# Performance work log

Hardware: AMD Instinct MI355X
Metric: run time of the kernel (lower is better)

The kernel has to match this reference:

```python
import jax, jax.numpy as jnp
import numpy as np

N, E, B = 128000, 512000, 128

def _conv1d(x, w, b):
    # x: [B,C,L], w: [O,I,K] (torch layout) -> valid conv, stride 1
    y = jax.lax.conv_general_dilated(x, w, (1,), 'VALID',
                                     dimension_numbers=('NCH', 'OIH', 'NCH'))
    return y + b[None, :, None]

def setup_inputs():
    key = jax.random.key(0)
    ks = jax.random.split(key, 22)
    def u(k, shape, fan_in):
        bound = 1.0 / np.sqrt(fan_in)
        return jax.random.uniform(k, shape, jnp.float32, -bound, bound)
    x = jax.random.normal(ks[0], (N, 33), jnp.float32)
    edge_index = jax.random.randint(ks[1], (2, E), 0, N, dtype=jnp.int64)
    batch = (jnp.arange(N, dtype=jnp.int64) * B) // N  # sorted, every graph non-empty
    target = jax.random.normal(ks[2], (B, 26, 1000), jnp.float32)
    return {
        'x': x, 'edge_index': edge_index, 'batch': batch, 'target': target,
        'lin_w': u(ks[3], (256, 33), 33), 'lin_b': jnp.zeros((256,), jnp.float32),
        'conv1_w': u(ks[4], (64, 26, 3), 26 * 3), 'conv1_b': u(ks[5], (64,), 26 * 3),
        'conv2_w': u(ks[6], (256, 64, 3), 64 * 3), 'conv2_b': u(ks[7], (256,), 64 * 3),
        'conv3_w': u(ks[8], (1024, 256, 5), 256 * 5), 'conv3_b': u(ks[9], (1024,), 256 * 5),
        'fc_w': u(ks[10], (768, 1024), 1024), 'fc_b': u(ks[11], (768,), 1024),
        'm1_w': u(ks[12], (1024, 1024), 1024), 'm1_b': u(ks[13], (1024,), 1024),
        'm2_w': u(ks[14], (1024, 1024), 1024), 'm2_b': u(ks[15], (1024,), 1024),
        'm3_w': u(ks[16], (512, 1024), 1024), 'm3_b': u(ks[17], (512,), 1024),
        'm4_w': u(ks[18], (1, 512), 512), 'm4_b': u(ks[19], (1,), 512),
    }

def reference(x, edge_index, batch, target,
              lin_w, lin_b, conv1_w, conv1_b, conv2_w, conv2_b,
              conv3_w, conv3_b, fc_w, fc_b,
              m1_w, m1_b, m2_w, m2_b, m3_w, m3_b, m4_w, m4_b):
    # ---- drug branch: GCN-normalized message passing, sum-aggr, graph mean ----
    xw = x @ lin_w.T                                   # [N,256]
    row, col = edge_index[0], edge_index[1]            # source j, target i
    deg = jax.ops.segment_sum(jnp.ones((E,), x.dtype), col, num_segments=N)
    dis = jnp.where(deg > 0, deg ** -0.5, 0.0)
    norm = dis[row] * dis[col]                         # [E]
    agg = jax.ops.segment_sum(norm[:, None] * xw[row], col, num_segments=N)
    out = agg + lin_b                                  # [N,256]
    sums = jax.ops.segment_sum(out, batch, num_segments=B)
    cnt = jax.ops.segment_sum(jnp.ones((N,), x.dtype), batch, num_segments=B)
    drug = jnp.where(cnt[:, None] > 0, sums / cnt[:, None], 0.0)  # [B,256]
    # ---- target branch: CNN (dropout = identity in eval) ----
    h = jax.nn.relu(_conv1d(target, conv1_w, conv1_b))
    h = jax.nn.relu(_conv1d(h, conv2_w, conv2_b))
    h = jax.nn.relu(_conv1d(h, conv3_w, conv3_b))
    h = jnp.max(h, axis=2)                             # AdaptiveMaxPool1d(1) -> [B,1024]
    tgt = jax.nn.relu(h @ fc_w.T + fc_b)               # [B,768]
    # ---- head MLP ----
    z = jnp.concatenate([drug, tgt], axis=1)           # [B,1024]
    z = jax.nn.relu(z @ m1_w.T + m1_b)
    z = jax.nn.relu(z @ m2_w.T + m2_b)
    z = jax.nn.relu(z @ m3_w.T + m3_b)
    return z @ m4_w.T + m4_b                           # [B,1]
```

## Files before the change

### kernel.cpp

```cpp
#include <hip/hip_runtime.h>

typedef unsigned short u16;
typedef __attribute__((ext_vector_type(8))) short short8;
typedef __attribute__((ext_vector_type(4))) float f32x4;

#define NN 128000
#define EE 512000
#define GB 128

#define GLDS16(g, l)                                                     \
  __builtin_amdgcn_global_load_lds(                                      \
      (const __attribute__((address_space(1))) unsigned int*)(g),        \
      (__attribute__((address_space(3))) unsigned int*)(l), 16, 0, 0)

__device__ __forceinline__ float u2f(u16 u) {
  union { unsigned u32; float f; } v; v.u32 = ((unsigned)u) << 16; return v.f;
}
__device__ __forceinline__ u16 f2bf(float x) {
  union { float f; unsigned u; } v; v.f = x;
  unsigned r = v.u + 0x7FFF + ((v.u >> 16) & 1);
  return (u16)(r >> 16);
}

__global__ void k_transpose(const float* w1, const float* w2, const float* w3,
                            float* w1T, u16* w2t, u16* w3p) {
  int idx = blockIdx.x * 256 + threadIdx.x;
  if (idx < 4992) { int o = idx & 63, ck = idx >> 6; w1T[idx] = w1[o * 78 + ck]; return; }
  idx -= 4992;
  if (idx < 49152) {
    int c = idx & 63, o = (idx >> 6) & 255, k = idx >> 14;
    w2t[idx] = f2bf(w2[o * 192 + c * 3 + k]);
    return;
  }
  idx -= 49152;
  if (idx < 1310720) {
    int stcbk = idx >> 15;
    int fi    = (idx >> 9) & 63;
    int r512  = idx & 511;
    int quad  = r512 >> 7, l16 = (r512 >> 3) & 15, i = r512 & 7;
    int stcb  = stcbk / 5, k = stcbk - stcb * 5;
    int o = fi * 16 + l16;
    int c = stcb * 32 + quad * 8 + i;
    w3p[idx] = f2bf(w3[o * 1280 + c * 5 + k]);
  }
}

__global__ void k_deg_start(const int* ei, const int* batch, int* deg, int* start, int* hist) {
  __shared__ int lh[GB];
  int tid = threadIdx.x, blk = blockIdx.x;
  if (tid < GB) lh[tid] = 0;
  __syncthreads();
  int e0 = blk * 1024;
#pragma unroll
  for (int t = 0; t < 4; t++) {
    int e = e0 + t * 256 + tid;
    int col = ei[EE + e];
    atomicAdd(&deg[col], 1);
    atomicAdd(&lh[batch[col]], 1);
  }
  int i = blk * 256 + tid;
  int b = batch[i];
  if (i == 0) start[0] = 0;
  else if (b != batch[i - 1]) start[b] = i;
  if (i == NN - 1) start[GB] = NN;
  __syncthreads();
  if (tid < GB && lh[tid]) atomicAdd(&hist[tid * 16], lh[tid]);
}

__global__ void k_prefix(const int* hist, int* off, int* cursor) {
  __shared__ int h[GB];
  int tid = threadIdx.x;
  h[tid] = hist[tid * 16];
  __syncthreads();
  int s = 0;
  for (int j = 0; j < tid; j++) s += h[j];
  off[tid] = s;
  cursor[tid * 16] = s;
  if (tid == GB - 1) off[GB] = s + h[GB - 1];
}

__global__ void k_scatter(const int* ei, const int* batch, const int* deg,
                          int* cursor, uint2* bucket) {
  __shared__ int lh[GB];
  __shared__ int lbase[GB];
  int tid = threadIdx.x, blk = blockIdx.x;
  if (tid < GB) lh[tid] = 0;
  __syncthreads();
  int e0 = blk * 1024;
  int row[4], g[4], rk[4]; float nrm[4];
#pragma unroll
  for (int t = 0; t < 4; t++) {
    int e = e0 + t * 256 + tid;
    int r = ei[e], c = ei[EE + e];
    row[t] = r;
    g[t] = batch[c];
    int dr = deg[r], dc = deg[c];
    float fr = dr > 0 ? rsqrtf((float)dr) : 0.f;
    float fc = dc > 0 ? rsqrtf((float)dc) : 0.f;
    nrm[t] = fr * fc;
    rk[t] = atomicAdd(&lh[g[t]], 1);
  }
  __syncthreads();
  if (tid < GB && lh[tid]) lbase[tid] = atomicAdd(&cursor[tid * 16], lh[tid]);
  __syncthreads();
#pragma unroll
  for (int t = 0; t < 4; t++) {
    uint2 v; v.x = (unsigned)row[t]; v.y = __float_as_uint(nrm[t]);
    bucket[lbase[g[t]] + rk[t]] = v;
  }
}

__global__ void k_gather33(const uint2* bucket, const int* off, const float* x, float* y) {
  __shared__ float red[4][33];
  int tid = threadIdx.x;
  int s = blockIdx.x, g = blockIdx.y;
  int lo = off[g], hi = off[g + 1];
  int cnt = hi - lo;
  int per = (cnt + 15) >> 4;
  int b0 = lo + s * per, b1 = min(b0 + per, hi);
  int lane = tid & 63, wid = tid >> 6;
  float acc = 0.f;
  if (lane < 33) {
#pragma unroll 4
    for (int e = b0 + wid; e < b1; e += 4) {
      uint2 be = bucket[e];
      float nrm = __uint_as_float(be.y);
      acc = fmaf(nrm, x[(size_t)be.x * 33 + lane], acc);
    }
    red[wid][lane] = acc;
  }
  __syncthreads();
  if (tid < 33) {
    float v = red[0][tid] + red[1][tid] + red[2][tid] + red[3][tid];
    if (v != 0.f) atomicAdd(&y[g * 33 + tid], v);
  }
}

__global__ void k_conv1(const float* target, const float* w1T, const float* b1, u16* h1T) {
  __shared__ float ts[26][132];
  __shared__ float wls[78 * 64];
  int tid = threadIdx.x, lt = blockIdx.x, bl = blockIdx.y;
  int l0 = lt * 128;
  int q = tid >> 6, lane = tid & 63;
  for (int c = q; c < 26; c += 4)
    for (int i = lane; i < 130; i += 64)
      ts[c][i] = target[(bl * 26 + c) * 1000 + min(l0 + i, 999)];
  for (int i = tid; i < 4992; i += 256) wls[i] = w1T[i];
  __syncthreads();
  int o = tid & 63, wid = tid >> 6;
  float w[78];
#pragma unroll
  for (int i = 0; i < 78; i++) w[i] = wls[i * 64 + o];
  float bias = b1[o];
  for (int t = 0; t < 32; t++) {
    int li = wid * 32 + t;
    float acc = bias;
#pragma unroll
    for (int c = 0; c < 26; c++)
#pragma unroll
      for (int k = 0; k < 3; k++) acc += ts[c][li + k] * w[c * 3 + k];
    int lg = l0 + li;
    if (lg < 998) h1T[((size_t)bl * 1000 + lg) * 64 + o] = f2bf(fmaxf(acc, 0.f));
  }
}

__global__ void k_conv2(const u16* h1T, const u16* w2t, const float* b2, u16* h2T) {
  __shared__ __align__(16) u16 als[132 * 32];
  __shared__ __align__(16) u16 bls[3 * 128 * 32];
  int tid = threadIdx.x;
  int lt = blockIdx.x, ot = blockIdx.y, bl = blockIdx.z;
  int l0 = lt * 128, o0 = ot * 128;
  int lane = tid & 63, wid = tid >> 6;
  int wm = wid >> 1, wn = wid & 1;
  int quad = lane >> 4, l16 = lane & 15;
  const f32x4 zero = {0.f, 0.f, 0.f, 0.f};
  f32x4 acc[4][4];
#pragma unroll
  for (int i = 0; i < 4; i++)
#pragma unroll
    for (int j = 0; j < 4; j++) acc[i][j] = zero;
  for (int cb = 0; cb < 2; cb++) {
    int c0 = cb * 32;
#pragma unroll
    for (int rr = 0; rr < 2; rr++) {
      int cid = rr * 256 + wid * 64 + lane;
      int row = cid >> 2, ch = (cid & 3) ^ (row & 3);
      GLDS16(h1T + ((size_t)bl * 1000 + min(l0 + row, 997)) * 64 + c0 + ch * 8,
             als + (rr * 256 + wid * 64) * 8);
    }
    if (wid == 0 && lane < 8) {
      int cid = 512 + lane;
      int row = cid >> 2, ch = (cid & 3) ^ (row & 3);
      GLDS16(h1T + ((size_t)bl * 1000 + min(l0 + row, 997)) * 64 + c0 + ch * 8, als + 512 * 8);
    }
#pragma unroll
    for (int rr = 0; rr < 6; rr++) {
      int cid = rr * 256 + wid * 64 + lane;
      int rko = cid >> 2, k = rko >> 7, o = rko & 127;
      int ch = (cid & 3) ^ (rko & 3);
      GLDS16(w2t + ((size_t)(k * 256 + o0 + o)) * 64 + c0 + ch * 8,
             bls + (rr * 256 + wid * 64) * 8);
    }
    __syncthreads();
#pragma unroll
    for (int k = 0; k < 3; k++) {
      short8 af[4], bfr[4];
#pragma unroll
      for (int i = 0; i < 4; i++) {
        int row = k + wm * 64 + i * 16 + l16;
        af[i] = *(const short8*)(als + row * 32 + ((quad ^ (row & 3)) * 8));
      }
#pragma unroll
      for (int j = 0; j < 4; j++) {
        int rowB = wn * 64 + j * 16 + l16;
        bfr[j] = *(const short8*)(bls + (k * 128 + rowB) * 32 + ((quad ^ (rowB & 3)) * 8));
      }
#pragma unroll
      for (int i = 0; i < 4; i++)
#pragma unroll
        for (int j = 0; j < 4; j++)
          acc[i][j] = __builtin_amdgcn_mfma_f32_16x16x32_bf16(af[i], bfr[j], acc[i][j], 0, 0, 0);
    }
    __syncthreads();
  }
#pragma unroll
  for (int j = 0; j < 4; j++) {
    int col = o0 + wn * 64 + j * 16 + l16;
    float bias = b2[col];
#pragma unroll
    for (int i = 0; i < 4; i++)
#pragma unroll
      for (int r = 0; r < 4; r++) {
        int lg = l0 + wm * 64 + i * 16 + quad * 4 + r;
        if (lg < 996)
          h2T[((size_t)bl * 996 + lg) * 256 + col] = f2bf(fmaxf(acc[i][j][r] + bias, 0.f));
      }
  }
}

__global__ void __launch_bounds__(256, 2)
k_conv3(const u16* h2T, const u16* w3p, const float* b3, float* pooledT) {
  __shared__ __align__(16) u16 als[2][1088 * 8];
  __shared__ float mbuf[256];
  int bid = blockIdx.x;
  int xc = bid & 7, rr0 = bid >> 3;
  int ot = rr0 & 3, bl = xc * 16 + (rr0 >> 2);
  int o0 = ot * 256;
  int tid = threadIdx.x;
  int lane = tid & 63, wn = tid >> 6;
  int quad = lane >> 4, l16 = lane & 15;
  float omax[4];
#pragma unroll
  for (int j = 0; j < 4; j++) omax[j] = -3.0e38f;
  const f32x4 zero = {0.f, 0.f, 0.f, 0.f};
  const u16* wb = w3p + (size_t)(ot * 16 + wn * 4) * 512 + lane * 8;
  const size_t rowbase = (size_t)bl * 996;

  {
    u16* dst = als[0];
#pragma unroll
    for (int c = 0; c < 4; c++) {
      int cid = c * 256 + tid;
      int row = cid >> 3, pp = cid & 7;
      int cc = (pp - row) & 7;
      GLDS16(h2T + (rowbase + min(row, 995)) * 256 + cc * 8, dst + cid * 8);
    }
    if (tid < 64) {
      int cid = 1024 + tid;
      int row = cid >> 3, pp = cid & 7;
      int cc = (pp - row) & 7;
      GLDS16(h2T + (rowbase + min(row, 995)) * 256 + cc * 8, dst + cid * 8);
    }
  }
  asm volatile("s_waitcnt vmcnt(0)" ::: "memory");
  __builtin_amdgcn_s_barrier();

  for (int lt = 0; lt < 8; lt++) {
    f32x4 acc[8][4];
#pragma unroll
    for (int i = 0; i < 8; i++)
#pragma unroll
      for (int j = 0; j < 4; j++) acc[i][j] = zero;
#pragma unroll 1
    for (int qc = 0; qc < 4; qc++) {
      const u16* a = als[qc & 1];
      {
        const u16* p_ = wb + (size_t)(qc * 2) * 5 * 32768;
        short8 breg[4];
        breg[0] = *(const short8*)(p_);
        breg[1] = *(const short8*)(p_ + 512);
        breg[2] = *(const short8*)(p_ + 1024);
        breg[3] = *(const short8*)(p_ + 1536);
#pragma unroll
        for (int i = 0; i < 8; i++) {
          int row = i * 16 + l16;
          int pp = (quad + row) & 7;
          short8 af = *(const short8*)(a + row * 64 + pp * 8);
          acc[i][0] = __builtin_amdgcn_mfma_f32_16x16x32_bf16(af, breg[0], acc[i][0], 0, 0, 0);
          acc[i][1] = __builtin_amdgcn_mfma_f32_16x16x32_bf16(af, breg[1], acc[i][1], 0, 0, 0);
          acc[i][2] = __builtin_amdgcn_mfma_f32_16x16x32_bf16(af, breg[2], acc[i][2], 0, 0, 0);
          acc[i][3] = __builtin_amdgcn_mfma_f32_16x16x32_bf16(af, breg[3], acc[i][3], 0, 0, 0);
        }
      }
      if (lt * 4 + qc < 31) {
        int nqc = (qc + 1) & 3;
        int nlt = lt + (qc == 3 ? 1 : 0);
        int l0n = nlt * 128;
        u16* dst = als[(qc + 1) & 1];
#pragma unroll
        for (int c = 0; c < 4; c++) {
          int cid = c * 256 + tid;
          int row = cid >> 3, pp = cid & 7;
          int cc = (pp - row) & 7;
          GLDS16(h2T + (rowbase + min(l0n + row, 995)) * 256 + nqc * 64 + cc * 8,
                 dst + cid * 8);
        }
        if (tid < 64) {
          int cid = 1024 + tid;
          int row = cid >> 3, pp = cid & 7;
          int cc = (pp - row) & 7;
          GLDS16(h2T + (rowbase + min(l0n + row, 995)) * 256 + nqc * 64 + cc * 8,
                 dst + cid * 8);
        }
      }
#pragma unroll 1
      for (int cbq = 0; cbq < 2; cbq++) {
        int stcb = qc * 2 + cbq;
        int k0 = (cbq == 0) ? 1 : 0;
#pragma unroll
        for (int k = k0; k < 5; k++) {
          const u16* p_ = wb + (size_t)(stcb * 5 + k) * 32768;
          short8 breg[4];
          breg[0] = *(const short8*)(p_);
          breg[1] = *(const short8*)(p_ + 512);
          breg[2] = *(const short8*)(p_ + 1024);
          breg[3] = *(const short8*)(p_ + 1536);
#pragma unroll
          for (int i = 0; i < 8; i++) {
            int row = k + i * 16 + l16;
            int pp = (cbq * 4 + quad + row) & 7;
            short8 af = *(const short8*)(a + row * 64 + pp * 8);
            acc[i][0] = __builtin_amdgcn_mfma_f32_16x16x32_bf16(af, breg[0], acc[i][0], 0, 0, 0);
            acc[i][1] = __builtin_amdgcn_mfma_f32_16x16x32_bf16(af, breg[1], acc[i][1], 0, 0, 0);
            acc[i][2] = __builtin_amdgcn_mfma_f32_16x16x32_bf16(af, breg[2], acc[i][2], 0, 0, 0);
            acc[i][3] = __builtin_amdgcn_mfma_f32_16x16x32_bf16(af, breg[3], acc[i][3], 0, 0, 0);
          }
        }
      }
      asm volatile("s_waitcnt vmcnt(0)" ::: "memory");
      __builtin_amdgcn_s_barrier();
    }
    int l0 = lt * 128;
#pragma unroll
    for (int i = 0; i < 8; i++) {
#pragma unroll
      for (int r = 0; r < 4; r++) {
        int lg = l0 + i * 16 + quad * 4 + r;
        if (lg < 992) {
#pragma unroll
          for (int j = 0; j < 4; j++) omax[j] = fmaxf(omax[j], acc[i][j][r]);
        }
      }
    }
  }
#pragma unroll
  for (int j = 0; j < 4; j++) {
    omax[j] = fmaxf(omax[j], __shfl_xor(omax[j], 16, 64));
    omax[j] = fmaxf(omax[j], __shfl_xor(omax[j], 32, 64));
  }
  if (quad == 0) {
#pragma unroll
    for (int j = 0; j < 4; j++) mbuf[wn * 64 + j * 16 + l16] = omax[j];
  }
  __syncthreads();
  {
    float v = mbuf[tid] + b3[o0 + tid];
    pooledT[(size_t)(o0 + tid) * 128 + bl] = fmaxf(v, 0.f);
  }
}

__global__ void k_z0(const float* y, const int* start, const float* lin_w, const float* lin_b,
                     const float* tgtT, float* z0T) {
  int idx = blockIdx.x * 256 + threadIdx.x;
  int r = idx >> 7, bb = idx & 127;
  float v;
  if (r < 256) {
    float cnt = (float)(start[bb + 1] - start[bb]);
    const float* yr = y + bb * 33;
    const float* wr = lin_w + r * 33;
    float acc = 0.f;
#pragma unroll
    for (int i = 0; i < 33; i++) acc = fmaf(yr[i], wr[i], acc);
    v = acc / cnt + lin_b[r];
  } else {
    v = tgtT[(r - 256) * 128 + bb];
  }
  z0T[idx] = v;
}

__global__ void k_fc4(const float* zT, const float* W, const float* bias, float* outT,
                      int K, int O) {
  __shared__ float wls[4 * 1024];
  int tid = threadIdx.x;
  int o0 = blockIdx.x * 4;
  for (int idx = tid; idx < 4 * K; idx += 512) {
    int oo = idx / K, i = idx - oo * K;
    wls[oo * K + i] = W[(size_t)(o0 + oo) * K + i];
  }
  __syncthreads();
  int osub = tid >> 7, bb = tid & 127;
  int o = o0 + osub;
  float acc = 0.f;
  const float* wp = &wls[osub * K];
#pragma unroll 8
  for (int i = 0; i < K; i++) acc = fmaf(wp[i], zT[i * 128 + bb], acc);
  acc += bias[o];
  outT[(size_t)o * 128 + bb] = fmaxf(acc, 0.f);
}

__global__ void k_fc_final(const float* zT, const float* W, const float* bias, float* final_out,
                           int K) {
  __shared__ float wls[512];
  int tid = threadIdx.x;
  for (int i = tid; i < K; i += 256) wls[i] = W[i];
  __syncthreads();
  if (tid >= 128) return;
  int bb = tid;
  float acc = 0.f;
#pragma unroll 8
  for (int i = 0; i < K; i++) acc = fmaf(wls[i], zT[i * 128 + bb], acc);
  final_out[bb] = acc + bias[0];
}

extern "C" void kernel_launch(void* const* d_in, const int* in_sizes, int n_in,
                              void* d_out, int out_size, void* d_ws, size_t ws_size,
                              hipStream_t stream) {
  const float* x      = (const float*)d_in[0];
  const int*   ei     = (const int*)d_in[1];
  const int*   batch  = (const int*)d_in[2];
  const float* target = (const float*)d_in[3];
  const float* lin_w  = (const float*)d_in[4];
  const float* lin_b  = (const float*)d_in[5];
  const float* w1     = (const float*)d_in[6];
  const float* b1     = (const float*)d_in[7];
  const float* w2     = (const float*)d_in[8];
  const float* b2     = (const float*)d_in[9];
  const float* w3     = (const float*)d_in[10];
  const float* b3     = (const float*)d_in[11];
  const float* fcw    = (const float*)d_in[12];
  const float* fcb    = (const float*)d_in[13];
  const float* m1w = (const float*)d_in[14]; const float* m1b = (const float*)d_in[15];
  const float* m2w = (const float*)d_in[16]; const float* m2b = (const float*)d_in[17];
  const float* m3w = (const float*)d_in[18]; const float* m3b = (const float*)d_in[19];
  const float* m4w = (const float*)d_in[20]; const float* m4b = (const float*)d_in[21];

  char* ws = (char*)d_ws;
  size_t ofs = 0;
  auto alloc = [&](size_t bytes) -> void* {
    void* p = ws + ofs;
    ofs = (ofs + bytes + 255) & ~(size_t)255;
    return p;
  };
  int*   deg    = (int*)alloc((size_t)NN * 4);
  int*   start  = (int*)alloc((size_t)(GB + 1) * 4);
  int*   hist   = (int*)alloc((size_t)GB * 16 * 4);
  int*   off    = (int*)alloc((size_t)(GB + 1) * 4);
  int*   cursor = (int*)alloc((size_t)GB * 16 * 4);
  uint2* bucket = (uint2*)alloc((size_t)EE * 8);
  float* y      = (float*)alloc((size_t)GB * 33 * 4);
  float* w1T    = (float*)alloc((size_t)78 * 64 * 4);
  u16*   w2t    = (u16*)alloc((size_t)3 * 256 * 64 * 2);
  u16*   w3p    = (u16*)alloc((size_t)5 * 1024 * 256 * 2);
  float* pooledT= (float*)alloc((size_t)1024 * 128 * 4);
  float* tgtT   = (float*)alloc((size_t)768 * 128 * 4);
  float* z0T    = (float*)alloc((size_t)1024 * 128 * 4);
  float* z1T    = (float*)alloc((size_t)1024 * 128 * 4);
  float* z2T    = (float*)alloc((size_t)1024 * 128 * 4);
  float* z3T    = (float*)alloc((size_t)512 * 128 * 4);
  size_t F_end = ofs;

  u16* h1T = (u16*)(ws + F_end);
  u16* h2T = (u16*)(ws + F_end + (size_t)128 * 1000 * 64 * 2);

  hipMemsetAsync(deg, 0, (size_t)NN * 4, stream);
  hipMemsetAsync(hist, 0, (size_t)GB * 16 * 4, stream);
  hipMemsetAsync(y, 0, (size_t)GB * 33 * 4, stream);

  k_transpose<<<5332, 256, 0, stream>>>(w1, w2, w3, w1T, w2t, w3p);
  k_deg_start<<<500, 256, 0, stream>>>(ei, batch, deg, start, hist);
  k_prefix<<<1, 128, 0, stream>>>(hist, off, cursor);
  k_scatter<<<500, 256, 0, stream>>>(ei, batch, deg, cursor, bucket);
  k_gather33<<<dim3(16, GB), 256, 0, stream>>>(bucket, off, x, y);

  k_conv1<<<dim3(8, 128), 256, 0, stream>>>(target, w1T, b1, h1T);
  k_conv2<<<dim3(8, 2, 128), 256, 0, stream>>>(h1T, w2t, b2, h2T);
  k_conv3<<<512, 256, 0, stream>>>(h2T, w3p, b3, pooledT);

  k_fc4<<<192, 512, 0, stream>>>(pooledT, fcw, fcb, tgtT, 1024, 768);
  k_z0<<<512, 256, 0, stream>>>(y, start, lin_w, lin_b, tgtT, z0T);
  k_fc4<<<256, 512, 0, stream>>>(z0T, m1w, m1b, z1T, 1024, 1024);
  k_fc4<<<256, 512, 0, stream>>>(z1T, m2w, m2b, z2T, 1024, 1024);
  k_fc4<<<128, 512, 0, stream>>>(z2T, m3w, m3b, z3T, 1024, 512);
  k_fc_final<<<1, 256, 0, stream>>>(z3T, m4w, m4b, (float*)d_out, 512);
}
```

Before: 738.9 us.

## Merge independent graph and CNN kernels into combined launches via block-index dispatch

Combines the degree/start pass with the weight transpose, the edge scatter with conv1, and the bucket gather with conv2 into single launches whose blocks branch on block index. Independent branches then share one grid, which removes three kernel launches and lets the small graph kernels run alongside the convolution work instead of serialising. In exchange each fused kernel takes the larger shared-memory and register footprint of both halves, which can lower occupancy for the lighter half. Interleaving gather blocks with conv2 blocks also changes how they are scheduled.

```diff
diff --git a/kernel.cpp b/kernel.cpp
--- a/kernel.cpp
+++ b/kernel.cpp
@@ -22,9 +22,33 @@
   return (u16)(r >> 16);
 }
 
-__global__ void k_transpose(const float* w1, const float* w2, const float* w3,
-                            float* w1T, u16* w2t, u16* w3p) {
-  int idx = blockIdx.x * 256 + threadIdx.x;
+__global__ void k_prep(const int* ei, const int* batch, int* deg, int* start, int* hist,
+                       const float* w1, const float* w2, const float* w3,
+                       float* w1T, u16* w2t, u16* w3p) {
+  __shared__ int lh[GB];
+  int tid = threadIdx.x, bid = blockIdx.x;
+  if (bid < 500) {
+    int blk = bid;
+    if (tid < GB) lh[tid] = 0;
+    __syncthreads();
+    int e0 = blk * 1024;
+#pragma unroll
+    for (int t = 0; t < 4; t++) {
+      int e = e0 + t * 256 + tid;
+      int col = ei[EE + e];
+      atomicAdd(&deg[col], 1);
+      atomicAdd(&lh[batch[col]], 1);
+    }
+    int i = blk * 256 + tid;
+    int b = batch[i];
+    if (i == 0) start[0] = 0;
+    else if (b != batch[i - 1]) start[b] = i;
+    if (i == NN - 1) start[GB] = NN;
+    __syncthreads();
+    if (tid < GB && lh[tid]) atomicAdd(&hist[tid * 16], lh[tid]);
+    return;
+  }
+  int idx = (bid - 500) * 256 + tid;
   if (idx < 4992) { int o = idx & 63, ck = idx >> 6; w1T[idx] = w1[o * 78 + ck]; return; }
   idx -= 4992;
   if (idx < 49152) {
@@ -45,28 +69,6 @@
   }
 }
 
-__global__ void k_deg_start(const int* ei, const int* batch, int* deg, int* start, int* hist) {
-  __shared__ int lh[GB];
-  int tid = threadIdx.x, blk = blockIdx.x;
-  if (tid < GB) lh[tid] = 0;
-  __syncthreads();
-  int e0 = blk * 1024;
-#pragma unroll
-  for (int t = 0; t < 4; t++) {
-    int e = e0 + t * 256 + tid;
-    int col = ei[EE + e];
-    atomicAdd(&deg[col], 1);
-    atomicAdd(&lh[batch[col]], 1);
-  }
-  int i = blk * 256 + tid;
-  int b = batch[i];
-  if (i == 0) start[0] = 0;
-  else if (b != batch[i - 1]) start[b] = i;
-  if (i == NN - 1) start[GB] = NN;
-  __syncthreads();
-  if (tid < GB && lh[tid]) atomicAdd(&hist[tid * 16], lh[tid]);
-}
-
 __global__ void k_prefix(const int* hist, int* off, int* cursor) {
   __shared__ int h[GB];
   int tid = threadIdx.x;
@@ -79,67 +81,45 @@
   if (tid == GB - 1) off[GB] = s + h[GB - 1];
 }
 
-__global__ void k_scatter(const int* ei, const int* batch, const int* deg,
-                          int* cursor, uint2* bucket) {
-  __shared__ int lh[GB];
-  __shared__ int lbase[GB];
-  int tid = threadIdx.x, blk = blockIdx.x;
-  if (tid < GB) lh[tid] = 0;
-  __syncthreads();
-  int e0 = blk * 1024;
-  int row[4], g[4], rk[4]; float nrm[4];
-#pragma unroll
-  for (int t = 0; t < 4; t++) {
-    int e = e0 + t * 256 + tid;
-    int r = ei[e], c = ei[EE + e];
-    row[t] = r;
-    g[t] = batch[c];
-    int dr = deg[r], dc = deg[c];
-    float fr = dr > 0 ? rsqrtf((float)dr) : 0.f;
-    float fc = dc > 0 ? rsqrtf((float)dc) : 0.f;
-    nrm[t] = fr * fc;
-    rk[t] = atomicAdd(&lh[g[t]], 1);
-  }
-  __syncthreads();
-  if (tid < GB && lh[tid]) lbase[tid] = atomicAdd(&cursor[tid * 16], lh[tid]);
-  __syncthreads();
-#pragma unroll
-  for (int t = 0; t < 4; t++) {
-    uint2 v; v.x = (unsigned)row[t]; v.y = __float_as_uint(nrm[t]);
-    bucket[lbase[g[t]] + rk[t]] = v;
-  }
-}
-
-__global__ void k_gather33(const uint2* bucket, const int* off, const float* x, float* y) {
-  __shared__ float red[4][33];
-  int tid = threadIdx.x;
-  int s = blockIdx.x, g = blockIdx.y;
-  int lo = off[g], hi = off[g + 1];
-  int cnt = hi - lo;
-  int per = (cnt + 15) >> 4;
-  int b0 = lo + s * per, b1 = min(b0 + per, hi);
-  int lane = tid & 63, wid = tid >> 6;
-  float acc = 0.f;
-  if (lane < 33) {
-#pragma unroll 4
-    for (int e = b0 + wid; e < b1; e += 4) {
-      uint2 be = bucket[e];
-      float nrm = __uint_as_float(be.y);
-      acc = fmaf(nrm, x[(size_t)be.x * 33 + lane], acc);
-    }
-    red[wid][lane] = acc;
-  }
-  __syncthreads();
-  if (tid < 33) {
-    float v = red[0][tid] + red[1][tid] + red[2][tid] + red[3][tid];
-    if (v != 0.f) atomicAdd(&y[g * 33 + tid], v);
-  }
-}
-
-__global__ void k_conv1(const float* target, const float* w1T, const float* b1, u16* h1T) {
-  __shared__ float ts[26][132];
-  __shared__ float wls[78 * 64];
-  int tid = threadIdx.x, lt = blockIdx.x, bl = blockIdx.y;
+__global__ void k_scatter_conv1(const int* ei, const int* batch, const int* deg, int* cursor,
+                                uint2* bucket, const float* target, const float* w1T,
+                                const float* b1, u16* h1T) {
+  __shared__ __align__(16) char smem[33696];
+  int tid = threadIdx.x, bid = blockIdx.x;
+  if (bid < 500) {
+    int* lh    = (int*)smem;
+    int* lbase = (int*)smem + GB;
+    int blk = bid;
+    if (tid < GB) lh[tid] = 0;
+    __syncthreads();
+    int e0 = blk * 1024;
+    int row[4], g[4], rk[4]; float nrm[4];
+#pragma unroll
+    for (int t = 0; t < 4; t++) {
+      int e = e0 + t * 256 + tid;
+      int r = ei[e], c = ei[EE + e];
+      row[t] = r;
+      g[t] = batch[c];
+      int dr = deg[r], dc = deg[c];
+      float fr = dr > 0 ? rsqrtf((float)dr) : 0.f;
+      float fc = dc > 0 ? rsqrtf((float)dc) : 0.f;
+      nrm[t] = fr * fc;
+      rk[t] = atomicAdd(&lh[g[t]], 1);
+    }
+    __syncthreads();
+    if (tid < GB && lh[tid]) lbase[tid] = atomicAdd(&cursor[tid * 16], lh[tid]);
+    __syncthreads();
+#pragma unroll
+    for (int t = 0; t < 4; t++) {
+      uint2 v; v.x = (unsigned)row[t]; v.y = __float_as_uint(nrm[t]);
+      bucket[lbase[g[t]] + rk[t]] = v;
+    }
+    return;
+  }
+  float (*ts)[132] = (float(*)[132])smem;
+  float* wls = (float*)(smem + 13728);
+  int id = bid - 500;
+  int lt = id & 7, bl = id >> 3;
   int l0 = lt * 128;
   int q = tid >> 6, lane = tid & 63;
   for (int c = q; c < 26; c += 4)
@@ -164,11 +144,40 @@
   }
 }
 
-__global__ void k_conv2(const u16* h1T, const u16* w2t, const float* b2, u16* h2T) {
-  __shared__ __align__(16) u16 als[132 * 32];
-  __shared__ __align__(16) u16 bls[3 * 128 * 32];
-  int tid = threadIdx.x;
-  int lt = blockIdx.x, ot = blockIdx.y, bl = blockIdx.z;
+__global__ void k_gather_conv2(const uint2* bucket, const int* off, const float* x, float* y,
+                               const u16* h1T, const u16* w2t, const float* b2, u16* h2T) {
+  __shared__ __align__(16) char smem[33024];
+  int tid = threadIdx.x, bid = blockIdx.x;
+  if (bid & 1) {
+    float (*red)[33] = (float(*)[33])smem;
+    int idx = bid >> 1;
+    int s = idx & 15, g = idx >> 4;
+    int lo = off[g], hi = off[g + 1];
+    int cnt = hi - lo;
+    int per = (cnt + 15) >> 4;
+    int b0 = lo + s * per, b1 = min(b0 + per, hi);
+    int lane = tid & 63, wid = tid >> 6;
+    float acc = 0.f;
+    if (lane < 33) {
+#pragma unroll 4
+      for (int e = b0 + wid; e < b1; e += 4) {
+        uint2 be = bucket[e];
+        float nrm = __uint_as_float(be.y);
+        acc = fmaf(nrm, x[(size_t)be.x * 33 + lane], acc);
+      }
+      red[wid][lane] = acc;
+    }
+    __syncthreads();
+    if (tid < 33) {
+      float v = red[0][tid] + red[1][tid] + red[2][tid] + red[3][tid];
+      if (v != 0.f) atomicAdd(&y[g * 33 + tid], v);
+    }
+    return;
+  }
+  u16* als = (u16*)smem;
+  u16* bls = (u16*)(smem + 8448);
+  int idx = bid >> 1;
+  int lt = idx & 7, ot = (idx >> 3) & 1, bl = idx >> 4;
   int l0 = lt * 128, o0 = ot * 128;
   int lane = tid & 63, wid = tid >> 6;
   int wm = wid >> 1, wn = wid & 1;
@@ -486,14 +495,11 @@
   hipMemsetAsync(hist, 0, (size_t)GB * 16 * 4, stream);
   hipMemsetAsync(y, 0, (size_t)GB * 33 * 4, stream);
 
-  k_transpose<<<5332, 256, 0, stream>>>(w1, w2, w3, w1T, w2t, w3p);
-  k_deg_start<<<500, 256, 0, stream>>>(ei, batch, deg, start, hist);
+  k_prep<<<5832, 256, 0, stream>>>(ei, batch, deg, start, hist, w1, w2, w3, w1T, w2t, w3p);
   k_prefix<<<1, 128, 0, stream>>>(hist, off, cursor);
-  k_scatter<<<500, 256, 0, stream>>>(ei, batch, deg, cursor, bucket);
-  k_gather33<<<dim3(16, GB), 256, 0, stream>>>(bucket, off, x, y);
-
-  k_conv1<<<dim3(8, 128), 256, 0, stream>>>(target, w1T, b1, h1T);
-  k_conv2<<<dim3(8, 2, 128), 256, 0, stream>>>(h1T, w2t, b2, h2T);
+  k_scatter_conv1<<<1524, 256, 0, stream>>>(ei, batch, deg, cursor, bucket,
+                                            target, w1T, b1, h1T);
+  k_gather_conv2<<<4096, 256, 0, stream>>>(bucket, off, x, y, h1T, w2t, b2, h2T);
   k_conv3<<<512, 256, 0, stream>>>(h2T, w3p, b3, pooledT);
 
   k_fc4<<<192, 512, 0, stream>>>(pooledT, fcw, fcb, tgtT, 1024, 768);
```

New measurement: 744.5 us. About the same (+0.8%).

## Restructure conv2 to keep weights in registers, full output width per block

Applied to the files above, without the earlier changes.

Conv2 weights are now pre-packed into an MFMA fragment layout, and each wave loads its B fragments straight from global memory into registers instead of staging them through LDS. Each block now computes all 256 output channels for a 128-position tile, so the activation tile is loaded into LDS once, with a rotated swizzle, and reused across all output channels. This removes the second grid dimension over output channels and the per-channel-block LDS syncs. In exchange each thread holds more accumulators, which raises register pressure, and the weights are read directly from global memory or cache.

```diff
diff --git a/kernel.cpp b/kernel.cpp
--- a/kernel.cpp
+++ b/kernel.cpp
@@ -23,13 +23,20 @@
 }
 
 __global__ void k_transpose(const float* w1, const float* w2, const float* w3,
-                            float* w1T, u16* w2t, u16* w3p) {
+                            float* w1T, u16* w2p, u16* w3p) {
   int idx = blockIdx.x * 256 + threadIdx.x;
   if (idx < 4992) { int o = idx & 63, ck = idx >> 6; w1T[idx] = w1[o * 78 + ck]; return; }
   idx -= 4992;
   if (idx < 49152) {
-    int c = idx & 63, o = (idx >> 6) & 255, k = idx >> 14;
-    w2t[idx] = f2bf(w2[o * 192 + c * 3 + k]);
+    int s    = idx >> 13;
+    int r    = idx & 8191;
+    int fi   = r >> 9;
+    int r512 = r & 511;
+    int quad = r512 >> 7, l16 = (r512 >> 3) & 15, i = r512 & 7;
+    int h = s / 3, tap = s - h * 3;
+    int o = fi * 16 + l16;
+    int c = h * 32 + quad * 8 + i;
+    w2p[idx] = f2bf(w2[o * 192 + c * 3 + tap]);
     return;
   }
   idx -= 49152;
@@ -164,74 +171,70 @@
   }
 }
 
-__global__ void k_conv2(const u16* h1T, const u16* w2t, const float* b2, u16* h2T) {
-  __shared__ __align__(16) u16 als[132 * 32];
-  __shared__ __align__(16) u16 bls[3 * 128 * 32];
+__global__ void __launch_bounds__(256, 2)
+k_conv2p(const u16* h1T, const u16* w2p, const float* b2, u16* h2T) {
+  __shared__ __align__(16) u16 als[1056 * 8];
+  int bid = blockIdx.x;
+  int xc = bid & 7, rr0 = bid >> 3;
+  int lt = rr0 & 7, bl = xc * 16 + (rr0 >> 3);
+  int l0 = lt * 128;
   int tid = threadIdx.x;
-  int lt = blockIdx.x, ot = blockIdx.y, bl = blockIdx.z;
-  int l0 = lt * 128, o0 = ot * 128;
-  int lane = tid & 63, wid = tid >> 6;
-  int wm = wid >> 1, wn = wid & 1;
+  int lane = tid & 63, wn = tid >> 6;
   int quad = lane >> 4, l16 = lane & 15;
   const f32x4 zero = {0.f, 0.f, 0.f, 0.f};
-  f32x4 acc[4][4];
-#pragma unroll
-  for (int i = 0; i < 4; i++)
+  f32x4 acc[8][4];
+#pragma unroll
+  for (int i = 0; i < 8; i++)
 #pragma unroll
     for (int j = 0; j < 4; j++) acc[i][j] = zero;
-  for (int cb = 0; cb < 2; cb++) {
-    int c0 = cb * 32;
-#pragma unroll
-    for (int rr = 0; rr < 2; rr++) {
-      int cid = rr * 256 + wid * 64 + lane;
-      int row = cid >> 2, ch = (cid & 3) ^ (row & 3);
-      GLDS16(h1T + ((size_t)bl * 1000 + min(l0 + row, 997)) * 64 + c0 + ch * 8,
-             als + (rr * 256 + wid * 64) * 8);
+  const u16* wb = w2p + (size_t)(wn * 4) * 512 + lane * 8;
+  const size_t rowbase = (size_t)bl * 1000;
+#pragma unroll
+  for (int c = 0; c < 4; c++) {
+    int cid = c * 256 + tid;
+    int row = cid >> 3, pp = cid & 7;
+    int cc = (pp - row) & 7;
+    GLDS16(h1T + (rowbase + min(l0 + row, 997)) * 64 + cc * 8, als + cid * 8);
+  }
+  if (tid < 32) {
+    int cid = 1024 + tid;
+    int row = cid >> 3, pp = cid & 7;
+    int cc = (pp - row) & 7;
+    GLDS16(h1T + (rowbase + min(l0 + row, 997)) * 64 + cc * 8, als + cid * 8);
+  }
+  asm volatile("s_waitcnt vmcnt(0)" ::: "memory");
+  __syncthreads();
+#pragma unroll 1
+  for (int h = 0; h < 2; h++) {
+#pragma unroll
+    for (int tap = 0; tap < 3; tap++) {
+      const u16* p_ = wb + (size_t)(h * 3 + tap) * 8192;
+      short8 breg[4];
+      breg[0] = *(const short8*)(p_);
+      breg[1] = *(const short8*)(p_ + 512);
+      breg[2] = *(const short8*)(p_ + 1024);
+      breg[3] = *(const short8*)(p_ + 1536);
+#pragma unroll
+      for (int i = 0; i < 8; i++) {
+        int row = tap + i * 16 + l16;
+        int pp = (h * 4 + quad + row) & 7;
+        short8 af = *(const short8*)(als + row * 64 + pp * 8);
+        acc[i][0] = __builtin_amdgcn_mfma_f32_16x16x32_bf16(af, breg[0], acc[i][0], 0, 0, 0);
+        acc[i][1] = __builtin_amdgcn_mfma_f32_16x16x32_bf16(af, breg[1], acc[i][1], 0, 0, 0);
+        acc[i][2] = __builtin_amdgcn_mfma_f32_16x16x32_bf16(af, breg[2], acc[i][2], 0, 0, 0);
+        acc[i][3] = __builtin_amdgcn_mfma_f32_16x16x32_bf16(af, breg[3], acc[i][3], 0, 0, 0);
+      }
     }
-    if (wid == 0 && lane < 8) {
-      int cid = 512 + lane;
-      int row = cid >> 2, ch = (cid & 3) ^ (row & 3);
-      GLDS16(h1T + ((size_t)bl * 1000 + min(l0 + row, 997)) * 64 + c0 + ch * 8, als + 512 * 8);
-    }
-#pragma unroll
-    for (int rr = 0; rr < 6; rr++) {
-      int cid = rr * 256 + wid * 64 + lane;
-      int rko = cid >> 2, k = rko >> 7, o = rko & 127;
-      int ch = (cid & 3) ^ (rko & 3);
-      GLDS16(w2t + ((size_t)(k * 256 + o0 + o)) * 64 + c0 + ch * 8,
-             bls + (rr * 256 + wid * 64) * 8);
-    }
-    __syncthreads();
-#pragma unroll
-    for (int k = 0; k < 3; k++) {
-      short8 af[4], bfr[4];
-#pragma unroll
-      for (int i = 0; i < 4; i++) {
-        int row = k + wm * 64 + i * 16 + l16;
-        af[i] = *(const short8*)(als + row * 32 + ((quad ^ (row & 3)) * 8));
-      }
-#pragma unroll
-      for (int j = 0; j < 4; j++) {
-        int rowB = wn * 64 + j * 16 + l16;
-        bfr[j] = *(const short8*)(bls + (k * 128 + rowB) * 32 + ((quad ^ (rowB & 3)) * 8));
-      }
-#pragma unroll
-      for (int i = 0; i < 4; i++)
-#pragma unroll
-        for (int j = 0; j < 4; j++)
-          acc[i][j] = __builtin_amdgcn_mfma_f32_16x16x32_bf16(af[i], bfr[j], acc[i][j], 0, 0, 0);
-    }
-    __syncthreads();
   }
 #pragma unroll
   for (int j = 0; j < 4; j++) {
-    int col = o0 + wn * 64 + j * 16 + l16;
+    int col = wn * 64 + j * 16 + l16;
     float bias = b2[col];
 #pragma unroll
-    for (int i = 0; i < 4; i++)
+    for (int i = 0; i < 8; i++)
 #pragma unroll
       for (int r = 0; r < 4; r++) {
-        int lg = l0 + wm * 64 + i * 16 + quad * 4 + r;
+        int lg = l0 + i * 16 + quad * 4 + r;
         if (lg < 996)
           h2T[((size_t)bl * 996 + lg) * 256 + col] = f2bf(fmaxf(acc[i][j][r] + bias, 0.f));
       }
@@ -469,7 +472,7 @@
   uint2* bucket = (uint2*)alloc((size_t)EE * 8);
   float* y      = (float*)alloc((size_t)GB * 33 * 4);
   float* w1T    = (float*)alloc((size_t)78 * 64 * 4);
-  u16*   w2t    = (u16*)alloc((size_t)3 * 256 * 64 * 2);
+  u16*   w2p    = (u16*)alloc((size_t)6 * 16 * 512 * 2);
   u16*   w3p    = (u16*)alloc((size_t)5 * 1024 * 256 * 2);
   float* pooledT= (float*)alloc((size_t)1024 * 128 * 4);
   float* tgtT   = (float*)alloc((size_t)768 * 128 * 4);
@@ -486,14 +489,14 @@
   hipMemsetAsync(hist, 0, (size_t)GB * 16 * 4, stream);
   hipMemsetAsync(y, 0, (size_t)GB * 33 * 4, stream);
 
-  k_transpose<<<5332, 256, 0, stream>>>(w1, w2, w3, w1T, w2t, w3p);
+  k_transpose<<<5332, 256, 0, stream>>>(w1, w2, w3, w1T, w2p, w3p);
   k_deg_start<<<500, 256, 0, stream>>>(ei, batch, deg, start, hist);
   k_prefix<<<1, 128, 0, stream>>>(hist, off, cursor);
   k_scatter<<<500, 256, 0, stream>>>(ei, batch, deg, cursor, bucket);
   k_gather33<<<dim3(16, GB), 256, 0, stream>>>(bucket, off, x, y);
 
   k_conv1<<<dim3(8, 128), 256, 0, stream>>>(target, w1T, b1, h1T);
-  k_conv2<<<dim3(8, 2, 128), 256, 0, stream>>>(h1T, w2t, b2, h2T);
+  k_conv2p<<<1024, 256, 0, stream>>>(h1T, w2p, b2, h2T);
   k_conv3<<<512, 256, 0, stream>>>(h2T, w3p, b3, pooledT);
 
   k_fc4<<<192, 512, 0, stream>>>(pooledT, fcw, fcb, tgtT, 1024, 768);
```

Result: no change. 736.5 us (-0.3%).
